# Performance work log

Measured on AMD Instinct MI355X. Metric: run time of the kernel, lower is better.

Reference implementation:

```python
import jax, jax.numpy as jnp
import numpy as np

VOCAB, EMB, HID, OUT = 100000, 300, 512, 1
B, SEQ = 1, 512


def setup_inputs() -> dict:
    key = jax.random.key(0)
    ks = jax.random.split(key, 8)
    s = 1.0 / np.sqrt(HID)  # torch LSTMCell/Linear init scale
    return {
        "x": jax.random.randint(ks[0], (B, SEQ), 0, VOCAB),
        "h0": jnp.zeros((B, HID), jnp.float32),
        "c0": jnp.zeros((B, HID), jnp.float32),
        "emb_table": jax.random.normal(ks[1], (VOCAB, EMB), jnp.float32) * 0.1,
        "W_ih": jax.random.uniform(ks[2], (4 * HID, EMB), jnp.float32, -s, s),
        "W_hh": jax.random.uniform(ks[3], (4 * HID, HID), jnp.float32, -s, s),
        "b_ih": jax.random.uniform(ks[4], (4 * HID,), jnp.float32, -s, s),
        "b_hh": jax.random.uniform(ks[5], (4 * HID,), jnp.float32, -s, s),
        "fc_w": jax.random.uniform(ks[6], (OUT, HID), jnp.float32, -s, s),
        "fc_b": jax.random.uniform(ks[7], (OUT,), jnp.float32, -s, s),
    }


def reference(x, h0, c0, emb_table, W_ih, W_hh, b_ih, b_hh, fc_w, fc_b):
    embeds = emb_table[x]                      # [B, SEQ, EMB]
    # Faithful to torch: embeds[0][i].view(B, EMB) for i in range(EMB); B == 1.
    steps = embeds[0, :EMB].reshape(EMB, B, EMB)  # [EMB steps, B, EMB]

    def cell(carry, xt):
        h, c = carry
        gates = xt @ W_ih.T + b_ih + h @ W_hh.T + b_hh   # [B, 4*HID]
        i, f, g, o = jnp.split(gates, 4, axis=-1)        # torch gate order i,f,g,o
        i = jax.nn.sigmoid(i)
        f = jax.nn.sigmoid(f)
        g = jnp.tanh(g)
        o = jax.nn.sigmoid(o)
        c = f * c + i * g
        h = o * jnp.tanh(c)
        return (h, c), None

    (h, c), _ = jax.lax.scan(cell, (h0, c0), steps)
    # dropout is identity in eval mode
    out = jax.nn.sigmoid(h @ fc_w.T + fc_b)   # [B, OUT]
    out = out.reshape(B, -1)[:, -1]           # [B]
    return (out, h, c)
```

## Files before the change

kernel.cpp:

```cpp
#include <hip/hip_runtime.h>

#define EMBD 300
#define NSTEP 300
#define HID 512
#define G4 2048
#define NWG 32
#define TPB 256

#define TS2 15
#define NSG 20
#define NRG 8

#define SENTINEL 0xFFC00000u

#define XP_SZ   (NSTEP * G4)
#define HSEQ_OFF XP_SZ

__device__ __forceinline__ float fsig(float x) { return 1.0f / (1.0f + __expf(-x)); }
__device__ __forceinline__ float ftanh(float x) {
    x = fminf(15.0f, fmaxf(-15.0f, x));
    float t = __expf(2.0f * x);
    return (t - 1.0f) / (t + 1.0f);
}

__global__ __launch_bounds__(TPB) void xproj_init_kernel(
    const int* __restrict__ x, const float* __restrict__ h0,
    const float* __restrict__ emb, const float* __restrict__ W_ih,
    const float* __restrict__ b_ih, const float* __restrict__ b_hh,
    float* __restrict__ ws) {
    const int rowg = blockIdx.x;
    const int sg   = blockIdx.y;
    const int tid  = threadIdx.x;
    const int t0   = sg * TS2;
    const int r    = rowg * TPB + tid;

    float* hseq = ws + HSEQ_OFF;

    if (rowg == 0) {
        unsigned* hs = (unsigned*)(hseq + (size_t)(t0 + 1) * HID);
        for (int i = tid; i < TS2 * HID; i += TPB) hs[i] = SENTINEL;
        if (sg == 0) {
            for (int i = tid; i < HID; i += TPB) hseq[i] = h0[i];
        }
    }

    __shared__ float e_lds[TS2][EMBD];
    for (int tt = 0; tt < TS2; ++tt) {
        const float* er = emb + (long long)x[t0 + tt] * EMBD;
        for (int i = tid; i < EMBD; i += TPB) e_lds[tt][i] = er[i];
    }
    __syncthreads();

    float acc[TS2];
    const float bsum = b_ih[r] + b_hh[r];
    #pragma unroll
    for (int tt = 0; tt < TS2; ++tt) acc[tt] = bsum;

    const float* wrow = W_ih + (size_t)r * EMBD;
    for (int e = 0; e < EMBD; e += 4) {
        const float4 w4 = *(const float4*)(wrow + e);
        #pragma unroll
        for (int tt = 0; tt < TS2; ++tt) {
            acc[tt] = fmaf(w4.x, e_lds[tt][e],     acc[tt]);
            acc[tt] = fmaf(w4.y, e_lds[tt][e + 1], acc[tt]);
            acc[tt] = fmaf(w4.z, e_lds[tt][e + 2], acc[tt]);
            acc[tt] = fmaf(w4.w, e_lds[tt][e + 3], acc[tt]);
        }
    }
    #pragma unroll
    for (int tt = 0; tt < TS2; ++tt)
        ws[(size_t)(t0 + tt) * G4 + r] = acc[tt];
}

__global__ __launch_bounds__(TPB, 1) void lstm_scan_kernel(
    const float* __restrict__ c0, const float* __restrict__ W_hh,
    const float* __restrict__ fc_w, const float* __restrict__ fc_b,
    float* __restrict__ ws, float* __restrict__ out) {
    const int tid  = threadIdx.x;
    const int wg   = blockIdx.x;
    const int v    = tid >> 6;
    const int lane = tid & 63;
    const int g    = lane >> 4;
    const int li   = lane & 15;
    const int hidx = wg * 16 + v * 4 + g;

    float* hseq    = ws + HSEQ_OFF;
    const float* xp = ws;

    __shared__ __align__(16) float h_lds[576];

    float wreg[4][32];
    #pragma unroll
    for (int gate = 0; gate < 4; ++gate) {
        const float* wr = W_hh + ((size_t)gate * HID + hidx) * HID + li * 32;
        #pragma unroll
        for (int k = 0; k < 32; k += 4) {
            const float4 w4 = *(const float4*)(wr + k);
            wreg[gate][k] = w4.x; wreg[gate][k + 1] = w4.y;
            wreg[gate][k + 2] = w4.z; wreg[gate][k + 3] = w4.w;
        }
    }

    const bool upd = (li == 0);
    float c = upd ? c0[hidx] : 0.0f;

    for (int s = 0; s < NSTEP; ++s) {
        float xi = 0.f, xf = 0.f, xg = 0.f, xo = 0.f;
        if (upd) {
            const float* xpt = xp + (size_t)s * G4 + hidx;
            xi = xpt[0]; xf = xpt[HID]; xg = xpt[2 * HID]; xo = xpt[3 * HID];
        }

        unsigned* hb = (unsigned*)(hseq + (size_t)s * HID);
        unsigned a = __hip_atomic_load(hb + tid,       __ATOMIC_RELAXED, __HIP_MEMORY_SCOPE_AGENT);
        unsigned b = __hip_atomic_load(hb + tid + 256, __ATOMIC_RELAXED, __HIP_MEMORY_SCOPE_AGENT);
        while (a == SENTINEL || b == SENTINEL) {
            __builtin_amdgcn_s_sleep(1);
            a = __hip_atomic_load(hb + tid,       __ATOMIC_RELAXED, __HIP_MEMORY_SCOPE_AGENT);
            b = __hip_atomic_load(hb + tid + 256, __ATOMIC_RELAXED, __HIP_MEMORY_SCOPE_AGENT);
        }
        const int i0 = tid, i1 = tid + 256;
        h_lds[i0 + ((i0 >> 5) << 2)] = __uint_as_float(a);
        h_lds[i1 + ((i1 >> 5) << 2)] = __uint_as_float(b);
        __syncthreads();

        float sums[4];
        const float* hrow = &h_lds[li * 36];
        #pragma unroll
        for (int gate = 0; gate < 4; ++gate) {
            float acc = 0.0f;
            #pragma unroll
            for (int k = 0; k < 32; k += 4) {
                const float4 h4 = *(const float4*)(hrow + k);
                acc = fmaf(wreg[gate][k],     h4.x, acc);
                acc = fmaf(wreg[gate][k + 1], h4.y, acc);
                acc = fmaf(wreg[gate][k + 2], h4.z, acc);
                acc = fmaf(wreg[gate][k + 3], h4.w, acc);
            }
            acc += __shfl_xor(acc, 1);
            acc += __shfl_xor(acc, 2);
            acc += __shfl_xor(acc, 4);
            acc += __shfl_xor(acc, 8);
            sums[gate] = acc;
        }

        if (upd) {
            const float iv = fsig(sums[0] + xi);
            const float fv = fsig(sums[1] + xf);
            const float gv = ftanh(sums[2] + xg);
            const float ov = fsig(sums[3] + xo);
            c = fv * c + iv * gv;
            const float h = ov * ftanh(c);
            __hip_atomic_store((unsigned*)(hseq + (size_t)(s + 1) * HID + hidx),
                               __float_as_uint(h),
                               __ATOMIC_RELAXED, __HIP_MEMORY_SCOPE_AGENT);
            if (s == NSTEP - 1) {
                out[1 + hidx] = h;
                out[1 + HID + hidx] = c;
            }
        }
        __syncthreads();
    }

    if (wg == 0) {
        __syncthreads();
        unsigned* hf = (unsigned*)(hseq + (size_t)NSTEP * HID);
        unsigned a = __hip_atomic_load(hf + tid,       __ATOMIC_RELAXED, __HIP_MEMORY_SCOPE_AGENT);
        unsigned b = __hip_atomic_load(hf + tid + 256, __ATOMIC_RELAXED, __HIP_MEMORY_SCOPE_AGENT);
        while (a == SENTINEL || b == SENTINEL) {
            __builtin_amdgcn_s_sleep(1);
            a = __hip_atomic_load(hf + tid,       __ATOMIC_RELAXED, __HIP_MEMORY_SCOPE_AGENT);
            b = __hip_atomic_load(hf + tid + 256, __ATOMIC_RELAXED, __HIP_MEMORY_SCOPE_AGENT);
        }
        float p = __uint_as_float(a) * fc_w[tid] + __uint_as_float(b) * fc_w[tid + 256];
        h_lds[tid] = p;
        __syncthreads();
        for (int off = 128; off > 0; off >>= 1) {
            if (tid < off) h_lds[tid] += h_lds[tid + off];
            __syncthreads();
        }
        if (tid == 0) out[0] = fsig(h_lds[0] + fc_b[0]);
    }
}

extern "C" void kernel_launch(void* const* d_in, const int* in_sizes, int n_in,
                              void* d_out, int out_size, void* d_ws, size_t ws_size,
                              hipStream_t stream) {
    (void)in_sizes; (void)n_in; (void)out_size; (void)ws_size;
    const int*   x     = (const int*)d_in[0];
    const float* h0    = (const float*)d_in[1];
    const float* c0    = (const float*)d_in[2];
    const float* emb   = (const float*)d_in[3];
    const float* W_ih  = (const float*)d_in[4];
    const float* W_hh  = (const float*)d_in[5];
    const float* b_ih  = (const float*)d_in[6];
    const float* b_hh  = (const float*)d_in[7];
    const float* fc_w  = (const float*)d_in[8];
    const float* fc_b  = (const float*)d_in[9];
    float* out = (float*)d_out;
    float* ws  = (float*)d_ws;

    xproj_init_kernel<<<dim3(NRG, NSG), dim3(TPB), 0, stream>>>(
        x, h0, emb, W_ih, b_ih, b_hh, ws);
    lstm_scan_kernel<<<dim3(NWG), dim3(TPB), 0, stream>>>(
        c0, W_hh, fc_w, fc_b, ws, out);
}
```

Baseline: 687.1 us.

## Confine LSTM scan workgroups to a single XCD and use sc0 polling

The scan kernel now launches 512 workgroups. Each one reads its XCC_ID and takes a slot in a per-XCD counter. The first XCD to gather 32 workgroups wins an election, and all other workgroups exit. This keeps the inter-workgroup h exchange inside one XCD's L2 so the per-step handoff avoids cross-die coherence latency. Polling switches to dwordx2 loads with sc0, falling back to an agent-scope atomic every eighth try, and producers write both sc0 and agent-scope stores. The trailing per-step __syncthreads is removed. The risks are launch overhead for many exiting workgroups, reliance on workgroup scheduling across XCDs, and possible LDS reuse hazards without the second barrier.

```diff
diff --git a/kernel.cpp b/kernel.cpp
--- a/kernel.cpp
+++ b/kernel.cpp
@@ -4,8 +4,9 @@
 #define NSTEP 300
 #define HID 512
 #define G4 2048
-#define NWG 32
 #define TPB 256
+#define NTEAM 32
+#define NWG_SCAN 512
 
 #define TS2 15
 #define NSG 20
@@ -13,14 +14,29 @@
 
 #define SENTINEL 0xFFC00000u
 
-#define XP_SZ   (NSTEP * G4)
+#define XP_SZ    (NSTEP * G4)
 #define HSEQ_OFF XP_SZ
+#define HSEQ_SZ  ((NSTEP + 1) * HID)
+#define ELECT_OFF (HSEQ_OFF + HSEQ_SZ)
 
 __device__ __forceinline__ float fsig(float x) { return 1.0f / (1.0f + __expf(-x)); }
 __device__ __forceinline__ float ftanh(float x) {
     x = fminf(15.0f, fmaxf(-15.0f, x));
     float t = __expf(2.0f * x);
     return (t - 1.0f) / (t + 1.0f);
+}
+
+__device__ __forceinline__ unsigned long long load2_sc0(const void* p) {
+    unsigned long long v;
+    asm volatile("global_load_dwordx2 %0, %1, off sc0\n\ts_waitcnt vmcnt(0)"
+                 : "=v"(v) : "v"(p) : "memory");
+    return v;
+}
+__device__ __forceinline__ void store1_sc0(void* p, unsigned v) {
+    asm volatile("global_store_dword %0, %1, off sc0" :: "v"(p), "v"(v) : "memory");
+}
+__device__ __forceinline__ bool has_sent(unsigned long long v) {
+    return ((unsigned)v == SENTINEL) || ((unsigned)(v >> 32) == SENTINEL);
 }
 
 __global__ __launch_bounds__(TPB) void xproj_init_kernel(
@@ -41,6 +57,10 @@
         for (int i = tid; i < TS2 * HID; i += TPB) hs[i] = SENTINEL;
         if (sg == 0) {
             for (int i = tid; i < HID; i += TPB) hseq[i] = h0[i];
+            if (tid < 16) {
+                unsigned* el = (unsigned*)(ws + ELECT_OFF);
+                el[tid] = (tid == 8) ? 0xFFFFFFFFu : 0u;
+            }
         }
     }
 
@@ -77,14 +97,46 @@
     const float* __restrict__ fc_w, const float* __restrict__ fc_b,
     float* __restrict__ ws, float* __restrict__ out) {
     const int tid  = threadIdx.x;
-    const int wg   = blockIdx.x;
+
+    __shared__ int s_slot;
+    __shared__ int s_win;
+
+    unsigned* el = (unsigned*)(ws + ELECT_OFF);
+    if (tid == 0) {
+        unsigned xcd;
+        asm volatile("s_getreg_b32 %0, hwreg(HW_REG_XCC_ID)" : "=s"(xcd));
+        xcd &= 7u;
+        const unsigned slot = __hip_atomic_fetch_add(&el[xcd], 1u,
+                                  __ATOMIC_RELAXED, __HIP_MEMORY_SCOPE_AGENT);
+        if (slot == NTEAM - 1) {
+            unsigned expect = 0xFFFFFFFFu;
+            __hip_atomic_compare_exchange_strong(&el[8], &expect, xcd,
+                __ATOMIC_RELAXED, __ATOMIC_RELAXED, __HIP_MEMORY_SCOPE_AGENT);
+        }
+        int win = 0, sl = -1;
+        if (slot < NTEAM) {
+            unsigned w;
+            do {
+                w = __hip_atomic_load(&el[8], __ATOMIC_RELAXED, __HIP_MEMORY_SCOPE_AGENT);
+                if (w == 0xFFFFFFFFu) __builtin_amdgcn_s_sleep(8);
+            } while (w == 0xFFFFFFFFu);
+            win = (w == xcd);
+            sl = (int)slot;
+        }
+        s_win = win;
+        s_slot = sl;
+    }
+    __syncthreads();
+    if (!s_win) return;
+    const int wg = s_slot;
+
     const int v    = tid >> 6;
     const int lane = tid & 63;
     const int g    = lane >> 4;
     const int li   = lane & 15;
     const int hidx = wg * 16 + v * 4 + g;
 
-    float* hseq    = ws + HSEQ_OFF;
+    float* hseq     = ws + HSEQ_OFF;
     const float* xp = ws;
 
     __shared__ __align__(16) float h_lds[576];
@@ -111,17 +163,21 @@
             xi = xpt[0]; xf = xpt[HID]; xg = xpt[2 * HID]; xo = xpt[3 * HID];
         }
 
-        unsigned* hb = (unsigned*)(hseq + (size_t)s * HID);
-        unsigned a = __hip_atomic_load(hb + tid,       __ATOMIC_RELAXED, __HIP_MEMORY_SCOPE_AGENT);
-        unsigned b = __hip_atomic_load(hb + tid + 256, __ATOMIC_RELAXED, __HIP_MEMORY_SCOPE_AGENT);
-        while (a == SENTINEL || b == SENTINEL) {
-            __builtin_amdgcn_s_sleep(1);
-            a = __hip_atomic_load(hb + tid,       __ATOMIC_RELAXED, __HIP_MEMORY_SCOPE_AGENT);
-            b = __hip_atomic_load(hb + tid + 256, __ATOMIC_RELAXED, __HIP_MEMORY_SCOPE_AGENT);
-        }
-        const int i0 = tid, i1 = tid + 256;
-        h_lds[i0 + ((i0 >> 5) << 2)] = __uint_as_float(a);
-        h_lds[i1 + ((i1 >> 5) << 2)] = __uint_as_float(b);
+        const unsigned* hb2 = (const unsigned*)(hseq + (size_t)s * HID) + 2 * tid;
+        unsigned long long hv = load2_sc0(hb2);
+        for (int k = 1; has_sent(hv); ++k) {
+            if ((k & 7) == 0)
+                hv = __hip_atomic_load((const unsigned long long*)hb2,
+                                       __ATOMIC_RELAXED, __HIP_MEMORY_SCOPE_AGENT);
+            else
+                hv = load2_sc0(hb2);
+        }
+        {
+            const int i0 = 2 * tid;
+            float2* dst = (float2*)&h_lds[i0 + ((i0 >> 5) << 2)];
+            *dst = make_float2(__uint_as_float((unsigned)hv),
+                               __uint_as_float((unsigned)(hv >> 32)));
+        }
         __syncthreads();
 
         float sums[4];
@@ -151,28 +207,31 @@
             const float ov = fsig(sums[3] + xo);
             c = fv * c + iv * gv;
             const float h = ov * ftanh(c);
-            __hip_atomic_store((unsigned*)(hseq + (size_t)(s + 1) * HID + hidx),
-                               __float_as_uint(h),
-                               __ATOMIC_RELAXED, __HIP_MEMORY_SCOPE_AGENT);
+            unsigned* dst = (unsigned*)(hseq + (size_t)(s + 1) * HID + hidx);
+            const unsigned hbits = __float_as_uint(h);
+            store1_sc0(dst, hbits);
+            __hip_atomic_store(dst, hbits, __ATOMIC_RELAXED,
+                               __HIP_MEMORY_SCOPE_AGENT);
             if (s == NSTEP - 1) {
                 out[1 + hidx] = h;
                 out[1 + HID + hidx] = c;
             }
         }
-        __syncthreads();
     }
 
     if (wg == 0) {
         __syncthreads();
-        unsigned* hf = (unsigned*)(hseq + (size_t)NSTEP * HID);
-        unsigned a = __hip_atomic_load(hf + tid,       __ATOMIC_RELAXED, __HIP_MEMORY_SCOPE_AGENT);
-        unsigned b = __hip_atomic_load(hf + tid + 256, __ATOMIC_RELAXED, __HIP_MEMORY_SCOPE_AGENT);
-        while (a == SENTINEL || b == SENTINEL) {
-            __builtin_amdgcn_s_sleep(1);
-            a = __hip_atomic_load(hf + tid,       __ATOMIC_RELAXED, __HIP_MEMORY_SCOPE_AGENT);
-            b = __hip_atomic_load(hf + tid + 256, __ATOMIC_RELAXED, __HIP_MEMORY_SCOPE_AGENT);
-        }
-        float p = __uint_as_float(a) * fc_w[tid] + __uint_as_float(b) * fc_w[tid + 256];
+        const unsigned* hf = (const unsigned*)(hseq + (size_t)NSTEP * HID);
+        unsigned long long va = load2_sc0(hf + 2 * tid);
+        for (int k = 1; has_sent(va); ++k) {
+            if ((k & 7) == 0)
+                va = __hip_atomic_load((const unsigned long long*)(hf + 2 * tid),
+                                       __ATOMIC_RELAXED, __HIP_MEMORY_SCOPE_AGENT);
+            else
+                va = load2_sc0(hf + 2 * tid);
+        }
+        const float p = __uint_as_float((unsigned)va) * fc_w[2 * tid]
+                      + __uint_as_float((unsigned)(va >> 32)) * fc_w[2 * tid + 1];
         h_lds[tid] = p;
         __syncthreads();
         for (int off = 128; off > 0; off >>= 1) {
@@ -202,6 +261,6 @@
 
     xproj_init_kernel<<<dim3(NRG, NSG), dim3(TPB), 0, stream>>>(
         x, h0, emb, W_ih, b_ih, b_hh, ws);
-    lstm_scan_kernel<<<dim3(NWG), dim3(TPB), 0, stream>>>(
+    lstm_scan_kernel<<<dim3(NWG_SCAN), dim3(TPB), 0, stream>>>(
         c0, W_hh, fc_w, fc_b, ws, out);
 }
```

Measured after the change: 1.159 ms. 1.69x slower.

## Replicate hidden-state mailboxes and poll with one wavefront using wide cache-bypassing loads

Applied to the files above, without the earlier changes.

Each step's hidden state is now written into 8 replicated mailbox copies, and each workgroup polls the copy chosen by its index. This spreads the contention on the polled cache lines across more lines. Only one wavefront per workgroup polls, using 32-byte global loads with sc0/sc1 bits and an occasional atomic fallback, and it drops the sleep. The per-step __syncthreads pairs become raw s_barrier calls, and the final FC reduction becomes a wave-level shuffle. In exchange there are 8 times more stores per step, a tighter spin loop, and a reliance on inline asm cache-coherence bits.

```diff
diff --git a/kernel.cpp b/kernel.cpp
--- a/kernel.cpp
+++ b/kernel.cpp
@@ -4,8 +4,9 @@
 #define NSTEP 300
 #define HID 512
 #define G4 2048
+#define TPB 256
 #define NWG 32
-#define TPB 256
+#define NMB 8
 
 #define TS2 15
 #define NSG 20
@@ -14,13 +15,48 @@
 #define SENTINEL 0xFFC00000u
 
 #define XP_SZ   (NSTEP * G4)
-#define HSEQ_OFF XP_SZ
+#define MB_OFF  XP_SZ
+#define MB_STEP (NMB * HID)
+
+typedef unsigned uint4v __attribute__((ext_vector_type(4)));
 
 __device__ __forceinline__ float fsig(float x) { return 1.0f / (1.0f + __expf(-x)); }
 __device__ __forceinline__ float ftanh(float x) {
     x = fminf(15.0f, fmaxf(-15.0f, x));
     float t = __expf(2.0f * x);
     return (t - 1.0f) / (t + 1.0f);
+}
+
+__device__ __forceinline__ void load32_sc(const void* p, uint4v& a, uint4v& b) {
+    asm volatile("global_load_dwordx4 %0, %2, off sc0 sc1\n\t"
+                 "global_load_dwordx4 %1, %2, off offset:16 sc0 sc1\n\t"
+                 "s_waitcnt vmcnt(0)"
+                 : "=v"(a), "=v"(b) : "v"(p) : "memory");
+}
+
+__device__ __forceinline__ bool any_sent(const uint4v& a, const uint4v& b) {
+    return a[0] == SENTINEL || a[1] == SENTINEL || a[2] == SENTINEL || a[3] == SENTINEL ||
+           b[0] == SENTINEL || b[1] == SENTINEL || b[2] == SENTINEL || b[3] == SENTINEL;
+}
+
+__device__ __forceinline__ void poll32(const float* p, uint4v& a, uint4v& b) {
+    load32_sc(p, a, b);
+    int k = 0;
+    while (any_sent(a, b)) {
+        if ((++k & 15) == 0) {
+            const unsigned long long* q = (const unsigned long long*)p;
+            unsigned long long q0 = __hip_atomic_load(q + 0, __ATOMIC_RELAXED, __HIP_MEMORY_SCOPE_AGENT);
+            unsigned long long q1 = __hip_atomic_load(q + 1, __ATOMIC_RELAXED, __HIP_MEMORY_SCOPE_AGENT);
+            unsigned long long q2 = __hip_atomic_load(q + 2, __ATOMIC_RELAXED, __HIP_MEMORY_SCOPE_AGENT);
+            unsigned long long q3 = __hip_atomic_load(q + 3, __ATOMIC_RELAXED, __HIP_MEMORY_SCOPE_AGENT);
+            a[0] = (unsigned)q0; a[1] = (unsigned)(q0 >> 32);
+            a[2] = (unsigned)q1; a[3] = (unsigned)(q1 >> 32);
+            b[0] = (unsigned)q2; b[1] = (unsigned)(q2 >> 32);
+            b[2] = (unsigned)q3; b[3] = (unsigned)(q3 >> 32);
+        } else {
+            load32_sc(p, a, b);
+        }
+    }
 }
 
 __global__ __launch_bounds__(TPB) void xproj_init_kernel(
@@ -34,13 +70,13 @@
     const int t0   = sg * TS2;
     const int r    = rowg * TPB + tid;
 
-    float* hseq = ws + HSEQ_OFF;
+    float* mb = ws + MB_OFF;
 
     if (rowg == 0) {
-        unsigned* hs = (unsigned*)(hseq + (size_t)(t0 + 1) * HID);
-        for (int i = tid; i < TS2 * HID; i += TPB) hs[i] = SENTINEL;
+        unsigned* msb = (unsigned*)(mb + (size_t)(t0 + 1) * MB_STEP);
+        for (int i = tid; i < TS2 * MB_STEP; i += TPB) msb[i] = SENTINEL;
         if (sg == 0) {
-            for (int i = tid; i < HID; i += TPB) hseq[i] = h0[i];
+            for (int i = tid; i < MB_STEP; i += TPB) mb[i] = h0[i & (HID - 1)];
         }
     }
 
@@ -83,8 +119,9 @@
     const int g    = lane >> 4;
     const int li   = lane & 15;
     const int hidx = wg * 16 + v * 4 + g;
-
-    float* hseq    = ws + HSEQ_OFF;
+    const int mbi  = wg & (NMB - 1);
+
+    float* mb       = ws + MB_OFF;
     const float* xp = ws;
 
     __shared__ __align__(16) float h_lds[576];
@@ -111,18 +148,19 @@
             xi = xpt[0]; xf = xpt[HID]; xg = xpt[2 * HID]; xo = xpt[3 * HID];
         }
 
-        unsigned* hb = (unsigned*)(hseq + (size_t)s * HID);
-        unsigned a = __hip_atomic_load(hb + tid,       __ATOMIC_RELAXED, __HIP_MEMORY_SCOPE_AGENT);
-        unsigned b = __hip_atomic_load(hb + tid + 256, __ATOMIC_RELAXED, __HIP_MEMORY_SCOPE_AGENT);
-        while (a == SENTINEL || b == SENTINEL) {
-            __builtin_amdgcn_s_sleep(1);
-            a = __hip_atomic_load(hb + tid,       __ATOMIC_RELAXED, __HIP_MEMORY_SCOPE_AGENT);
-            b = __hip_atomic_load(hb + tid + 256, __ATOMIC_RELAXED, __HIP_MEMORY_SCOPE_AGENT);
-        }
-        const int i0 = tid, i1 = tid + 256;
-        h_lds[i0 + ((i0 >> 5) << 2)] = __uint_as_float(a);
-        h_lds[i1 + ((i1 >> 5) << 2)] = __uint_as_float(b);
-        __syncthreads();
+        if (v == 0) {
+            const float* src = mb + (size_t)s * MB_STEP + (size_t)mbi * HID + lane * 8;
+            uint4v a, b;
+            poll32(src, a, b);
+            const int i0 = lane * 8;
+            float4* dst = (float4*)&h_lds[i0 + ((i0 >> 5) << 2)];
+            dst[0] = make_float4(__uint_as_float(a[0]), __uint_as_float(a[1]),
+                                 __uint_as_float(a[2]), __uint_as_float(a[3]));
+            dst[1] = make_float4(__uint_as_float(b[0]), __uint_as_float(b[1]),
+                                 __uint_as_float(b[2]), __uint_as_float(b[3]));
+        }
+        asm volatile("s_waitcnt lgkmcnt(0)" ::: "memory");
+        __builtin_amdgcn_s_barrier();
 
         float sums[4];
         const float* hrow = &h_lds[li * 36];
@@ -144,42 +182,51 @@
             sums[gate] = acc;
         }
 
+        float hnew = 0.0f;
         if (upd) {
             const float iv = fsig(sums[0] + xi);
             const float fv = fsig(sums[1] + xf);
             const float gv = ftanh(sums[2] + xg);
             const float ov = fsig(sums[3] + xo);
             c = fv * c + iv * gv;
-            const float h = ov * ftanh(c);
-            __hip_atomic_store((unsigned*)(hseq + (size_t)(s + 1) * HID + hidx),
-                               __float_as_uint(h),
-                               __ATOMIC_RELAXED, __HIP_MEMORY_SCOPE_AGENT);
+            hnew = ov * ftanh(c);
             if (s == NSTEP - 1) {
-                out[1 + hidx] = h;
+                out[1 + hidx] = hnew;
                 out[1 + HID + hidx] = c;
             }
         }
-        __syncthreads();
-    }
-
-    if (wg == 0) {
-        __syncthreads();
-        unsigned* hf = (unsigned*)(hseq + (size_t)NSTEP * HID);
-        unsigned a = __hip_atomic_load(hf + tid,       __ATOMIC_RELAXED, __HIP_MEMORY_SCOPE_AGENT);
-        unsigned b = __hip_atomic_load(hf + tid + 256, __ATOMIC_RELAXED, __HIP_MEMORY_SCOPE_AGENT);
-        while (a == SENTINEL || b == SENTINEL) {
-            __builtin_amdgcn_s_sleep(1);
-            a = __hip_atomic_load(hf + tid,       __ATOMIC_RELAXED, __HIP_MEMORY_SCOPE_AGENT);
-            b = __hip_atomic_load(hf + tid + 256, __ATOMIC_RELAXED, __HIP_MEMORY_SCOPE_AGENT);
-        }
-        float p = __uint_as_float(a) * fc_w[tid] + __uint_as_float(b) * fc_w[tid + 256];
-        h_lds[tid] = p;
-        __syncthreads();
-        for (int off = 128; off > 0; off >>= 1) {
-            if (tid < off) h_lds[tid] += h_lds[tid + off];
-            __syncthreads();
-        }
-        if (tid == 0) out[0] = fsig(h_lds[0] + fc_b[0]);
+        const float h0v = __shfl(hnew, 0);
+        const float h1v = __shfl(hnew, 16);
+        const float h2v = __shfl(hnew, 32);
+        const float h3v = __shfl(hnew, 48);
+        if (lane < 8) {
+            float* dst = mb + (size_t)(s + 1) * MB_STEP + (size_t)lane * HID
+                       + wg * 16 + v * 4;
+            __hip_atomic_store(dst + 0, h0v, __ATOMIC_RELAXED, __HIP_MEMORY_SCOPE_AGENT);
+            __hip_atomic_store(dst + 1, h1v, __ATOMIC_RELAXED, __HIP_MEMORY_SCOPE_AGENT);
+            __hip_atomic_store(dst + 2, h2v, __ATOMIC_RELAXED, __HIP_MEMORY_SCOPE_AGENT);
+            __hip_atomic_store(dst + 3, h3v, __ATOMIC_RELAXED, __HIP_MEMORY_SCOPE_AGENT);
+        }
+        __builtin_amdgcn_sched_barrier(0);
+        __builtin_amdgcn_s_barrier();
+    }
+
+    if (wg == 0 && v == 0) {
+        const float* src = mb + (size_t)NSTEP * MB_STEP + lane * 8;
+        uint4v a, b;
+        poll32(src, a, b);
+        const float* fw = fc_w + lane * 8;
+        float p = __uint_as_float(a[0]) * fw[0] + __uint_as_float(a[1]) * fw[1]
+                + __uint_as_float(a[2]) * fw[2] + __uint_as_float(a[3]) * fw[3]
+                + __uint_as_float(b[0]) * fw[4] + __uint_as_float(b[1]) * fw[5]
+                + __uint_as_float(b[2]) * fw[6] + __uint_as_float(b[3]) * fw[7];
+        p += __shfl_xor(p, 1);
+        p += __shfl_xor(p, 2);
+        p += __shfl_xor(p, 4);
+        p += __shfl_xor(p, 8);
+        p += __shfl_xor(p, 16);
+        p += __shfl_xor(p, 32);
+        if (lane == 0) out[0] = fsig(p + fc_b[0]);
     }
 }
 
```

After: 828.0 us. 20.5% more time.

## Replace sleep-based h polling with pipelined 64-bit inline-asm spin loads

Applied to the files above, without the earlier changes.

Each thread now polls one 64-bit pair of the previous hidden state with four outstanding cache-bypassing global loads in an inline-asm loop, with no sleep. Producers pack two adjacent h values through a lane shuffle and publish them with a single 64-bit atomic store, so no pair is seen half-written. The trailing per-step __syncthreads is dropped. This targets the cross-workgroup handoff latency of the sequential 300-step scan, at the cost of more memory traffic from busy polling and reliance on hand-written asm correctness.

```diff
diff --git a/kernel.cpp b/kernel.cpp
--- a/kernel.cpp
+++ b/kernel.cpp
@@ -4,16 +4,17 @@
 #define NSTEP 300
 #define HID 512
 #define G4 2048
+#define TPB 256
 #define NWG 32
-#define TPB 256
 
 #define TS2 15
 #define NSG 20
 #define NRG 8
 
 #define SENTINEL 0xFFC00000u
-
-#define XP_SZ   (NSTEP * G4)
+#define SENT64   0xFFC00000FFC00000ull
+
+#define XP_SZ    (NSTEP * G4)
 #define HSEQ_OFF XP_SZ
 
 __device__ __forceinline__ float fsig(float x) { return 1.0f / (1.0f + __expf(-x)); }
@@ -21,6 +22,49 @@
     x = fminf(15.0f, fmaxf(-15.0f, x));
     float t = __expf(2.0f * x);
     return (t - 1.0f) / (t + 1.0f);
+}
+
+__device__ __forceinline__ unsigned long long poll8_pipe(const void* p,
+                                                         unsigned long long sen) {
+    unsigned long long r0, r1, r2, r3;
+    asm volatile(
+        "global_load_dwordx2 %[r0], %[ad], off sc0 sc1\n\t"
+        "global_load_dwordx2 %[r1], %[ad], off sc0 sc1\n\t"
+        "global_load_dwordx2 %[r2], %[ad], off sc0 sc1\n\t"
+        "global_load_dwordx2 %[r3], %[ad], off sc0 sc1\n"
+        "LP%=:\n\t"
+        "s_waitcnt vmcnt(3)\n\t"
+        "v_cmp_eq_u64 vcc, %[sn], %[r0]\n\t"
+        "s_cbranch_vccz G0%=\n\t"
+        "global_load_dwordx2 %[r0], %[ad], off sc0 sc1\n\t"
+        "s_waitcnt vmcnt(3)\n\t"
+        "v_cmp_eq_u64 vcc, %[sn], %[r1]\n\t"
+        "s_cbranch_vccz G1%=\n\t"
+        "global_load_dwordx2 %[r1], %[ad], off sc0 sc1\n\t"
+        "s_waitcnt vmcnt(3)\n\t"
+        "v_cmp_eq_u64 vcc, %[sn], %[r2]\n\t"
+        "s_cbranch_vccz G2%=\n\t"
+        "global_load_dwordx2 %[r2], %[ad], off sc0 sc1\n\t"
+        "s_waitcnt vmcnt(3)\n\t"
+        "v_cmp_eq_u64 vcc, %[sn], %[r3]\n\t"
+        "s_cbranch_vccz G3%=\n\t"
+        "global_load_dwordx2 %[r3], %[ad], off sc0 sc1\n\t"
+        "s_branch LP%=\n"
+        "G3%=:\n\t"
+        "v_lshlrev_b64 %[r0], 0, %[r3]\n\t"
+        "s_branch GE%=\n"
+        "G2%=:\n\t"
+        "v_lshlrev_b64 %[r0], 0, %[r2]\n\t"
+        "s_branch GE%=\n"
+        "G1%=:\n\t"
+        "v_lshlrev_b64 %[r0], 0, %[r1]\n"
+        "GE%=:\n"
+        "G0%=:\n\t"
+        "s_waitcnt vmcnt(0)"
+        : [r0] "=&v"(r0), [r1] "=&v"(r1), [r2] "=&v"(r2), [r3] "=&v"(r3)
+        : [ad] "v"(p), [sn] "v"(sen)
+        : "vcc", "memory");
+    return r0;
 }
 
 __global__ __launch_bounds__(TPB) void xproj_init_kernel(
@@ -84,7 +128,7 @@
     const int li   = lane & 15;
     const int hidx = wg * 16 + v * 4 + g;
 
-    float* hseq    = ws + HSEQ_OFF;
+    float* hseq     = ws + HSEQ_OFF;
     const float* xp = ws;
 
     __shared__ __align__(16) float h_lds[576];
@@ -111,17 +155,14 @@
             xi = xpt[0]; xf = xpt[HID]; xg = xpt[2 * HID]; xo = xpt[3 * HID];
         }
 
-        unsigned* hb = (unsigned*)(hseq + (size_t)s * HID);
-        unsigned a = __hip_atomic_load(hb + tid,       __ATOMIC_RELAXED, __HIP_MEMORY_SCOPE_AGENT);
-        unsigned b = __hip_atomic_load(hb + tid + 256, __ATOMIC_RELAXED, __HIP_MEMORY_SCOPE_AGENT);
-        while (a == SENTINEL || b == SENTINEL) {
-            __builtin_amdgcn_s_sleep(1);
-            a = __hip_atomic_load(hb + tid,       __ATOMIC_RELAXED, __HIP_MEMORY_SCOPE_AGENT);
-            b = __hip_atomic_load(hb + tid + 256, __ATOMIC_RELAXED, __HIP_MEMORY_SCOPE_AGENT);
-        }
-        const int i0 = tid, i1 = tid + 256;
-        h_lds[i0 + ((i0 >> 5) << 2)] = __uint_as_float(a);
-        h_lds[i1 + ((i1 >> 5) << 2)] = __uint_as_float(b);
+        const unsigned long long hv =
+            poll8_pipe((const float*)hseq + (size_t)s * HID + 2 * tid, SENT64);
+        {
+            const int i0 = 2 * tid;
+            float2* dst = (float2*)&h_lds[i0 + ((i0 >> 5) << 2)];
+            *dst = make_float2(__uint_as_float((unsigned)hv),
+                               __uint_as_float((unsigned)(hv >> 32)));
+        }
         __syncthreads();
 
         float sums[4];
@@ -144,35 +185,36 @@
             sums[gate] = acc;
         }
 
+        float hnew = 0.0f;
         if (upd) {
             const float iv = fsig(sums[0] + xi);
             const float fv = fsig(sums[1] + xf);
             const float gv = ftanh(sums[2] + xg);
             const float ov = fsig(sums[3] + xo);
             c = fv * c + iv * gv;
-            const float h = ov * ftanh(c);
-            __hip_atomic_store((unsigned*)(hseq + (size_t)(s + 1) * HID + hidx),
-                               __float_as_uint(h),
-                               __ATOMIC_RELAXED, __HIP_MEMORY_SCOPE_AGENT);
+            hnew = ov * ftanh(c);
             if (s == NSTEP - 1) {
-                out[1 + hidx] = h;
+                out[1 + hidx] = hnew;
                 out[1 + HID + hidx] = c;
             }
         }
+        const float hpart = __shfl(hnew, lane + 16);
+        if (upd && (g & 1) == 0) {
+            const unsigned long long pair =
+                (unsigned long long)__float_as_uint(hnew) |
+                ((unsigned long long)__float_as_uint(hpart) << 32);
+            unsigned long long* dst = (unsigned long long*)
+                (hseq + (size_t)(s + 1) * HID + wg * 16 + v * 4 + g);
+            __hip_atomic_store(dst, pair, __ATOMIC_RELAXED, __HIP_MEMORY_SCOPE_AGENT);
+        }
+    }
+
+    if (wg == 0) {
+        const unsigned long long va =
+            poll8_pipe((const float*)hseq + (size_t)NSTEP * HID + 2 * tid, SENT64);
+        const float p = __uint_as_float((unsigned)va) * fc_w[2 * tid]
+                      + __uint_as_float((unsigned)(va >> 32)) * fc_w[2 * tid + 1];
         __syncthreads();
-    }
-
-    if (wg == 0) {
-        __syncthreads();
-        unsigned* hf = (unsigned*)(hseq + (size_t)NSTEP * HID);
-        unsigned a = __hip_atomic_load(hf + tid,       __ATOMIC_RELAXED, __HIP_MEMORY_SCOPE_AGENT);
-        unsigned b = __hip_atomic_load(hf + tid + 256, __ATOMIC_RELAXED, __HIP_MEMORY_SCOPE_AGENT);
-        while (a == SENTINEL || b == SENTINEL) {
-            __builtin_amdgcn_s_sleep(1);
-            a = __hip_atomic_load(hf + tid,       __ATOMIC_RELAXED, __HIP_MEMORY_SCOPE_AGENT);
-            b = __hip_atomic_load(hf + tid + 256, __ATOMIC_RELAXED, __HIP_MEMORY_SCOPE_AGENT);
-        }
-        float p = __uint_as_float(a) * fc_w[tid] + __uint_as_float(b) * fc_w[tid + 256];
         h_lds[tid] = p;
         __syncthreads();
         for (int off = 128; off > 0; off >>= 1) {
```

Measured after the change: 831.8 us. +21.1%, slower.
